# Kernel tuning notes

Measured on AMD Instinct MI355X. Metric: run time of the kernel, lower is better.

## Reference

```python
import jax, jax.numpy as jnp
import numpy as np

N = 16384        # num nodes
NE = 262144      # num edges (avg degree 16)
IN = 3           # input_dim
H = 128          # hidden_dim
ED = 2           # edge_dim (position differences, 2D coords)
L = 3            # num GNN layers
LAT = 64         # latent_dim
NR = 8192        # num reduced nodes (reduction_factor=0.5)
K = 3            # kNN for interpolation


def _ln(x, g, b, eps=1e-5):
    m = jnp.mean(x, axis=-1, keepdims=True)
    v = jnp.mean((x - m) ** 2, axis=-1, keepdims=True)
    return (x - m) / jnp.sqrt(v + eps) * g + b


def _mlp(x, w1, b1, w2, b2):
    return jax.nn.relu(x @ w1 + b1) @ w2 + b2


def setup_inputs() -> dict:
    key = jax.random.key(0)
    ks = jax.random.split(key, 32)
    def nrm(k, shape, s=0.05):
        return jax.random.normal(k, shape, dtype=jnp.float32) * s
    inp = {}
    inp["x"] = jax.random.normal(ks[0], (N, IN), dtype=jnp.float32)
    inp["node_positions"] = jax.random.uniform(ks[1], (N, 2), dtype=jnp.float32)
    inp["edge_index"] = jax.random.randint(ks[2], (2, NE), 0, N, dtype=jnp.int32)
    # mlp0 + lnm0
    inp["m0_w1"] = nrm(ks[3], (IN, H)); inp["m0_b1"] = jnp.zeros((H,), jnp.float32)
    inp["m0_w2"] = nrm(ks[4], (H, H)); inp["m0_b2"] = jnp.zeros((H,), jnp.float32)
    inp["ln0_g"] = jnp.ones((H,), jnp.float32); inp["ln0_b"] = jnp.zeros((H,), jnp.float32)
    # mlp1 + lnm1 (edge feature transform, edge_dim=2)
    inp["m1_w1"] = nrm(ks[5], (ED, H)); inp["m1_b1"] = jnp.zeros((H,), jnp.float32)
    inp["m1_w2"] = nrm(ks[6], (H, ED)); inp["m1_b2"] = jnp.zeros((ED,), jnp.float32)
    inp["ln1_g"] = jnp.ones((ED,), jnp.float32); inp["ln1_b"] = jnp.zeros((ED,), jnp.float32)
    # GNN layers (stacked over L)
    inp["g_msg_w1"] = nrm(ks[7], (L, 2 * H + ED, H)); inp["g_msg_b1"] = jnp.zeros((L, H), jnp.float32)
    inp["g_msg_w2"] = nrm(ks[8], (L, H, H)); inp["g_msg_b2"] = jnp.zeros((L, H), jnp.float32)
    inp["g_node_w1"] = nrm(ks[9], (L, 2 * H, H)); inp["g_node_b1"] = jnp.zeros((L, H), jnp.float32)
    inp["g_node_w2"] = nrm(ks[10], (L, H, H)); inp["g_node_b2"] = jnp.zeros((L, H), jnp.float32)
    inp["g_edge_w1"] = nrm(ks[11], (L, 2 * H + ED, H)); inp["g_edge_b1"] = jnp.zeros((L, H), jnp.float32)
    inp["g_edge_w2"] = nrm(ks[12], (L, H, ED)); inp["g_edge_b2"] = jnp.zeros((L, ED), jnp.float32)
    inp["g_lnn_g"] = jnp.ones((L, H), jnp.float32); inp["g_lnn_b"] = jnp.zeros((L, H), jnp.float32)
    inp["g_lne_g"] = jnp.ones((L, ED), jnp.float32); inp["g_lne_b"] = jnp.zeros((L, ED), jnp.float32)
    # mlp2 + lnm2
    inp["m2_w1"] = nrm(ks[13], (H, H)); inp["m2_b1"] = jnp.zeros((H,), jnp.float32)
    inp["m2_w2"] = nrm(ks[14], (H, H)); inp["m2_b2"] = jnp.zeros((H,), jnp.float32)
    inp["ln2_g"] = jnp.ones((H,), jnp.float32); inp["ln2_b"] = jnp.zeros((H,), jnp.float32)
    # output_proj
    inp["op_w1"] = nrm(ks[15], (H, H)); inp["op_b1"] = jnp.zeros((H,), jnp.float32)
    inp["op_w2"] = nrm(ks[16], (H, LAT)); inp["op_b2"] = jnp.zeros((LAT,), jnp.float32)
    return inp


def reference(x, edge_index, node_positions,
              m0_w1, m0_b1, m0_w2, m0_b2, ln0_g, ln0_b,
              m1_w1, m1_b1, m1_w2, m1_b2, ln1_g, ln1_b,
              g_msg_w1, g_msg_b1, g_msg_w2, g_msg_b2,
              g_node_w1, g_node_b1, g_node_w2, g_node_b2,
              g_edge_w1, g_edge_b1, g_edge_w2, g_edge_b2,
              g_lnn_g, g_lnn_b, g_lne_g, g_lne_b,
              m2_w1, m2_b1, m2_w2, m2_b2, ln2_g, ln2_b,
              op_w1, op_b1, op_w2, op_b2):
    row, col = edge_index[0], edge_index[1]
    # Stage 1: node encoder  U0 -> U1
    u = _ln(_mlp(x, m0_w1, m0_b1, m0_w2, m0_b2), ln0_g, ln0_b)
    # Stage 2: edge features from positions, E0 -> E1
    e = node_positions[col] - node_positions[row]          # [NE, 2]
    e = _ln(_mlp(e, m1_w1, m1_b1, m1_w2, m1_b2), ln1_g, ln1_b)
    # Stage 3: message-passing layers
    ones = jnp.ones((NE, 1), dtype=u.dtype)
    cnt = jnp.maximum(jax.ops.segment_sum(ones, col, num_segments=N), 1.0)
    for l in range(L):
        msg_in = jnp.concatenate([u[row], u[col], e], axis=-1)   # [NE, 2H+ED]
        m = _mlp(msg_in, g_msg_w1[l], g_msg_b1[l], g_msg_w2[l], g_msg_b2[l])
        agg = jax.ops.segment_sum(m, col, num_segments=N) / cnt  # mean aggregation
        u = _ln(u + _mlp(jnp.concatenate([u, agg], axis=-1),
                         g_node_w1[l], g_node_b1[l], g_node_w2[l], g_node_b2[l]),
                g_lnn_g[l], g_lnn_b[l])
        e = _ln(e + _mlp(jnp.concatenate([u[row], u[col], e], axis=-1),
                         g_edge_w1[l], g_edge_b1[l], g_edge_w2[l], g_edge_b2[l]),
                g_lne_g[l], g_lne_b[l])
    # Stage 4: U2 -> U3
    u3 = _ln(_mlp(u, m2_w1, m2_b1, m2_w2, m2_b2), ln2_g, ln2_b)
    # Stage 5: interpolate onto reduced coordinates (kNN inverse-distance weights)
    idx_r = jnp.floor(jnp.linspace(0.0, N - 1, NR)).astype(jnp.int32)
    x2 = node_positions[idx_r]                               # [NR, 2]
    d2 = (jnp.sum(x2 * x2, axis=1)[:, None]
          + jnp.sum(node_positions * node_positions, axis=1)[None, :]
          - 2.0 * x2 @ node_positions.T)                     # [NR, N]
    d2 = jnp.maximum(d2, 0.0)
    neg_d2, knn = jax.lax.top_k(-d2, K)                      # [NR, K]
    w = 1.0 / (jnp.sqrt(-neg_d2) + 1e-8)
    w = w / jnp.sum(w, axis=1, keepdims=True)
    z_feat = jnp.einsum('nk,nkh->nh', w, u3[knn])            # [NR, H]
    # Stage 6: global mean pool (no batch vector) + output projection
    z = jnp.mean(z_feat, axis=0, keepdims=True)              # [1, H]
    return _mlp(z, op_w1, op_b1, op_w2, op_b2)               # [1, LAT]
```

## Files before the change

kernel.cpp:

```cpp
#include <hip/hip_runtime.h>
#include <cfloat>

#define NN     16384
#define NEDGE  262144
#define HD     128
#define NLAYER 3
#define NRED   8192
#define LATD   64
#define GDIM   32

typedef __attribute__((ext_vector_type(8))) short short8;
typedef __attribute__((ext_vector_type(4))) float f32x4;

__device__ __forceinline__ unsigned short f2bf(float f) {
    union { float f; unsigned u; } v; v.f = f;
    unsigned u = v.u;
    unsigned r = u + 0x7fff + ((u >> 16) & 1);
    return (unsigned short)(r >> 16);
}
__device__ __forceinline__ void unp8(uint4 v, float* f) {
    unsigned w0=v.x, w1=v.y, w2=v.z, w3=v.w;
    f[0]=__uint_as_float(w0<<16); f[1]=__uint_as_float(w0&0xffff0000u);
    f[2]=__uint_as_float(w1<<16); f[3]=__uint_as_float(w1&0xffff0000u);
    f[4]=__uint_as_float(w2<<16); f[5]=__uint_as_float(w2&0xffff0000u);
// ... 113 lines not shown
        short8 a0 = *(const short8*)&HU.Hs[ 0 + lr][ks*32 + lq*8];
        short8 a1 = *(const short8*)&HU.Hs[16 + lr][ks*32 + lq*8];
        short8 a2 = *(const short8*)&HU.Hs[32 + lr][ks*32 + lq*8];
        short8 a3 = *(const short8*)&HU.Hs[48 + lr][ks*32 + lq*8];
        short8 b0 = *(const short8*)(W2p + (size_t)(((wave*2+0)*4 + ks)*64 + lane)*8);
        short8 b1v= *(const short8*)(W2p + (size_t)(((wave*2+1)*4 + ks)*64 + lane)*8);
        acc[0] = __builtin_amdgcn_mfma_f32_16x16x32_bf16(a0, b0, acc[0], 0,0,0);
        acc[1] = __builtin_amdgcn_mfma_f32_16x16x32_bf16(a0, b1v, acc[1], 0,0,0);
        acc[2] = __builtin_amdgcn_mfma_f32_16x16x32_bf16(a1, b0, acc[2], 0,0,0);
        acc[3] = __builtin_amdgcn_mfma_f32_16x16x32_bf16(a1, b1v, acc[3], 0,0,0);
        acc[4] = __builtin_amdgcn_mfma_f32_16x16x32_bf16(a2, b0, acc[4], 0,0,0);
        acc[5] = __builtin_amdgcn_mfma_f32_16x16x32_bf16(a2, b1v, acc[5], 0,0,0);
        acc[6] = __builtin_amdgcn_mfma_f32_16x16x32_bf16(a3, b0, acc[6], 0,0,0);
        acc[7] = __builtin_amdgcn_mfma_f32_16x16x32_bf16(a3, b1v, acc[7], 0,0,0);
    }
    #pragma unroll
    for (int b = 0; b < 2; ++b) {
        int n = (wave*2 + b)*16 + lr;
        float bb = B2[n];
        #pragma unroll
        for (int mt = 0; mt < 4; ++mt) {
            f32x4 v = acc[mt*2 + b];
            #pragma unroll
            for (int r = 0; r < 4; ++r) {
                int m = mt*16 + lq*4 + r;
                Rs[m][n] = v[r] + bb;
            }
        }
    }
    __syncthreads();
    {
        int m = tid >> 2, p = tid & 3;
        float s = 0.f;
        #pragma unroll 8
        for (int i = 0; i < 32; ++i) s += Rs[m][p*32 + i];
        red[m][p] = s;
    }
    __syncthreads();
    if (tid < 64) mstat[tid] = (red[tid][0]+red[tid][1]+red[tid][2]+red[tid][3]) * (1.f/HD);
    __syncthreads();
    {
        int m = tid >> 2, p = tid & 3;
        float mm = mstat[m];
        float s = 0.f;
        #pragma unroll 8
        for (int i = 0; i < 32; ++i) { float d = Rs[m][p*32 + i] - mm; s += d*d; }
        red[m][p] = s;
    }
    __syncthreads();
    if (tid < 64) sstat[tid] = sqrtf((red[tid][0]+red[tid][1]+red[tid][2]+red[tid][3]) * (1.f/HD) + 1e-5f);
    __syncthreads();
    for (int t = tid; t < 2048; t += 256) {
        int m = t >> 5, q = t & 31;
        int n = q*4;
        float mm = mstat[m], sd = sstat[m];
        float4 g4 = *(const float4*)(lg + n);
        float4 b4 = *(const float4*)(lb + n);
        float o0 = (Rs[m][n+0]-mm)/sd*g4.x + b4.x;
        float o1 = (Rs[m][n+1]-mm)/sd*g4.y + b4.y;
        float o2 = (Rs[m][n+2]-mm)/sd*g4.z + b4.z;
        float o3 = (Rs[m][n+3]-mm)/sd*g4.w + b4.w;
        float4 fo; fo.x=o0; fo.y=o1; fo.z=o2; fo.w=o3;
        *(float4*)(u + (size_t)(n0+m)*HD + n) = fo;
        uint2 pk; pk.x = f2bf(o0) | (f2bf(o1)<<16); pk.y = f2bf(o2) | (f2bf(o3)<<16);
        *(uint2*)(u16 + (size_t)(n0+m)*HD + n) = pk;
        int ksf = n >> 5, sub = (n >> 3) & 3;
        int slot = (ksf*4 + (m >> 4))*64 + ((m & 15) | (sub << 4));
        unsigned short* UF = (unsigned short*)HU.UF4;
        *(uint2*)&UF[slot*8 + (n & 7)] = pk;
    }
    __syncthreads();

    for (int g = 0; g < 2; ++g) {
        int ksOff = g*4;
        unsigned short* Out = g ? CM : RM;
        #pragma unroll
        for (int i = 0; i < 8; ++i) acc[i] = (f32x4){0.f,0.f,0.f,0.f};
        for (int ks = 0; ks < 4; ++ks) {
            short8 a0 = *(const short8*)&HU.UF4[(ks*4+0)*64 + lane];
            short8 a1 = *(const short8*)&HU.UF4[(ks*4+1)*64 + lane];
            short8 a2 = *(const short8*)&HU.UF4[(ks*4+2)*64 + lane];
            short8 a3 = *(const short8*)&HU.UF4[(ks*4+3)*64 + lane];
            short8 b0 = *(const short8*)(mW1p + (size_t)(((wave*2+0)*8 + ksOff + ks)*64 + lane)*8);
            short8 b1v= *(const short8*)(mW1p + (size_t)(((wave*2+1)*8 + ksOff + ks)*64 + lane)*8);
            acc[0] = __builtin_amdgcn_mfma_f32_16x16x32_bf16(a0, b0, acc[0], 0,0,0);
            acc[1] = __builtin_amdgcn_mfma_f32_16x16x32_bf16(a0, b1v, acc[1], 0,0,0);
            acc[2] = __builtin_amdgcn_mfma_f32_16x16x32_bf16(a1, b0, acc[2], 0,0,0);
            acc[3] = __builtin_amdgcn_mfma_f32_16x16x32_bf16(a1, b1v, acc[3], 0,0,0);
            acc[4] = __builtin_amdgcn_mfma_f32_16x16x32_bf16(a2, b0, acc[4], 0,0,0);
            acc[5] = __builtin_amdgcn_mfma_f32_16x16x32_bf16(a2, b1v, acc[5], 0,0,0);
            acc[6] = __builtin_amdgcn_mfma_f32_16x16x32_bf16(a3, b0, acc[6], 0,0,0);
            acc[7] = __builtin_amdgcn_mfma_f32_16x16x32_bf16(a3, b1v, acc[7], 0,0,0);
        }
        #pragma unroll
        for (int b = 0; b < 2; ++b) {
            int n = (wave*2 + b)*16 + lr;
            float bb = g ? mB1[n] : 0.f;
            #pragma unroll
            for (int mt = 0; mt < 4; ++mt) {
                f32x4 v = acc[mt*2 + b];
                #pragma unroll
                for (int r = 0; r < 4; ++r) {
                    int rowp = n0 + mt*16 + lq*4 + r;
                    unsigned hv = f2bf(v[r] + bb);
                    unsigned ph = (unsigned)__shfl_xor((int)hv, 1, 64);
                    if (!(lr & 1))
                        *(unsigned*)&Out[(size_t)rowp*HD + n] = hv | (ph << 16);
                }
            }
        }
    }
}

__global__ __launch_bounds__(256) void k_edge_enc(
    const float* __restrict__ pos, const int* __restrict__ row, const int* __restrict__ col,
    const float* __restrict__ w1, const float* __restrict__ b1,
    const float* __restrict__ w2, const float* __restrict__ b2,
    const float* __restrict__ lg, const float* __restrict__ lb,
    float* __restrict__ ef)
{
    int e = blockIdx.x*256 + threadIdx.x;
    if (e >= NEDGE) return;
    int r = row[e], c = col[e];
    float e0 = pos[c*2]   - pos[r*2];
    float e1 = pos[c*2+1] - pos[r*2+1];
    float o0 = b2[0], o1 = b2[1];
    for (int j = 0; j < HD; ++j) {
        float h = fmaxf(e0*w1[j] + e1*w1[HD+j] + b1[j], 0.f);
        o0 += h*w2[j*2];
        o1 += h*w2[j*2+1];
    }
    float m  = 0.5f*(o0 + o1);
    float d0 = o0 - m, d1 = o1 - m;
    float v  = 0.5f*(d0*d0 + d1*d1);
    float sd = sqrtf(v + 1e-5f);
    ef[e*2]   = d0/sd*lg[0] + lb[0];
    ef[e*2+1] = d1/sd*lg[1] + lb[1];
}

__global__ void k_count2(const int* __restrict__ col, const float* __restrict__ pos,
                         int* __restrict__ cnt, int* __restrict__ gcnt)
{
    int e = blockIdx.x*256 + threadIdx.x;
    if (e < NEDGE) atomicAdd(&cnt[col[e]], 1);
    if (e < NN) {
        int cx = min(max((int)(pos[e*2]  *(float)GDIM), 0), GDIM-1);
        int cy = min(max((int)(pos[e*2+1]*(float)GDIM), 0), GDIM-1);
        atomicAdd(&gcnt[cy*GDIM + cx], 1);
    }
}

__global__ __launch_bounds__(256) void k_scan2(
    const int* __restrict__ cnt, int* __restrict__ head,
    const int* __restrict__ gcnt, int* __restrict__ gstart, int* __restrict__ ghead,
    float* __restrict__ zsum)
{
    __shared__ int ls[257];
    int tid = threadIdx.x;
    if (blockIdx.x == 0) {
        int base = tid * (NN/256);
        int s = 0;
        for (int i = 0; i < NN/256; ++i) s += cnt[base + i];
        ls[tid+1] = s;
        if (tid == 0) ls[0] = 0;
        __syncthreads();
        if (tid == 0) for (int i = 1; i <= 256; ++i) ls[i] += ls[i-1];
        __syncthreads();
        int run = ls[tid];
        for (int i = 0; i < NN/256; ++i) {
            head[base + i] = run;
            run += cnt[base + i];
        }
    } else {
        if (tid < HD) zsum[tid] = 0.f;
        int base = tid * 4;
        int s = 0;
        for (int i = 0; i < 4; ++i) s += gcnt[base + i];
        ls[tid+1] = s;
        if (tid == 0) ls[0] = 0;
        __syncthreads();
        if (tid == 0) for (int i = 1; i <= 256; ++i) ls[i] += ls[i-1];
        __syncthreads();
        int run = ls[tid];
        for (int i = 0; i < 4; ++i) {
            gstart[base+i] = run; ghead[base+i] = run;
            run += gcnt[base+i];
        }
        if (tid == 255) gstart[GDIM*GDIM] = run;
    }
}

__global__ __launch_bounds__(256) void k_scatter2(
    const int* __restrict__ col, const float* __restrict__ pos,
    int* __restrict__ head, int* __restrict__ perm,
    int* __restrict__ ghead, float2* __restrict__ psort, int* __restrict__ pidx)
{
    int e = blockIdx.x*256 + threadIdx.x;
    if (e < NEDGE) {
        int p = atomicAdd(&head[col[e]], 1);
        perm[p] = e;
    }
    if (e < NN) {
        float px = pos[e*2], py = pos[e*2+1];
        int cx = min(max((int)(px*(float)GDIM), 0), GDIM-1);
        int cy = min(max((int)(py*(float)GDIM), 0), GDIM-1);
        int p = atomicAdd(&ghead[cy*GDIM + cx], 1);
        float2 pp; pp.x = px; pp.y = py;
        psort[p] = pp;
        pidx[p] = e;
    }
}

__global__ __launch_bounds__(256) void k_knnsel(
    const float* __restrict__ pos, const int* __restrict__ gstart,
    const float2* __restrict__ psort, const int* __restrict__ pidx,
    int* __restrict__ knnidx, float* __restrict__ knnw)
{
    int r = blockIdx.x*256 + threadIdx.x;
    int ni = (int)(2.0*r + (double)r/8191.0);
    float qx = pos[ni*2], qy = pos[ni*2+1];
    float s2 = qx*qx + qy*qy;
    int cx = min(max((int)(qx*(float)GDIM), 0), GDIM-1);
    int cy = min(max((int)(qy*(float)GDIM), 0), GDIM-1);
    const float h = 1.f/(float)GDIM;
    unsigned long long k0 = ~0ull, k1 = ~0ull, k2 = ~0ull;
    for (int rr = 0; rr < GDIM; ++rr) {
        if (rr > 0 && k2 != ~0ull) {
            float bound = rr*h;
            float d3 = __uint_as_float((unsigned)(k2 >> 32));
            if (d3 < bound*bound*0.9999f) break;
        }
        int ylo = max(cy-rr, 0), yhi = min(cy+rr, GDIM-1);
        int xlo = max(cx-rr, 0), xhi = min(cx+rr, GDIM-1);
        for (int gy = ylo; gy <= yhi; ++gy) {
            bool yedge = (gy == cy-rr) || (gy == cy+rr);
            for (int gx = xlo; gx <= xhi; ++gx) {
                if (!yedge && gx != cx-rr && gx != cx+rr) continue;
                int cell = gy*GDIM + gx;
                int s = gstart[cell], e = gstart[cell+1];
                for (; s < e; ++s) {
                    float2 p = psort[s];
                    float sc = p.x*p.x + p.y*p.y;
                    float dt = qx*p.x + qy*p.y;
                    float d2 = fmaxf(s2 + sc - 2.f*dt, 0.f);
                    unsigned long long key =
                        ((unsigned long long)__float_as_uint(d2) << 32) | (unsigned)pidx[s];
                    unsigned long long a0 = umin64(k0, key);
                    unsigned long long a1 = umin64(k1, umax64(k0, key));
                    unsigned long long a2 = umin64(k2, umax64(k1, key));
                    k0 = a0; k1 = a1; k2 = a2;
                }
            }
        }
    }
    float d0 = __uint_as_float((unsigned)(k0 >> 32));
    float d1 = __uint_as_float((unsigned)(k1 >> 32));
    float d2 = __uint_as_float((unsigned)(k2 >> 32));
    float w0 = 1.f/(sqrtf(d0) + 1e-8f);
    float w1 = 1.f/(sqrtf(d1) + 1e-8f);
    float w2 = 1.f/(sqrtf(d2) + 1e-8f);
    float ws = w0 + w1 + w2;
    knnidx[r*3+0] = (int)(unsigned)(k0 & 0xffffffffu);
    knnidx[r*3+1] = (int)(unsigned)(k1 & 0xffffffffu);
    knnidx[r*3+2] = (int)(unsigned)(k2 & 0xffffffffu);
    knnw[r*3+0] = w0/ws;
    knnw[r*3+1] = w1/ws;
    knnw[r*3+2] = w2/ws;
}

__global__ __launch_bounds__(256) void k_gather(
    const float* __restrict__ u3, const int* __restrict__ knnidx,
    const float* __restrict__ knnw, float* __restrict__ zsum)
{
    __shared__ float zp[HD];
    int tid = threadIdx.x;
    if (tid < HD) zp[tid] = 0.f;
    __syncthreads();
    int lane = tid & 63, w = tid >> 6;
    int q = blockIdx.x*4 + w;
    int i0 = knnidx[q*3], i1 = knnidx[q*3+1], i2 = knnidx[q*3+2];
    float w0 = knnw[q*3], w1 = knnw[q*3+1], w2 = knnw[q*3+2];
    const float* r0 = u3 + (size_t)i0*HD;
    const float* r1 = u3 + (size_t)i1*HD;
    const float* r2 = u3 + (size_t)i2*HD;
    for (int c = lane; c < HD; c += 64) {
        float v = w0*r0[c] + w1*r1[c] + w2*r2[c];
        atomicAdd(&zp[c], v);
    }
    __syncthreads();
    if (tid < HD) atomicAdd(&zsum[tid], zp[tid]);
}

__global__ __launch_bounds__(256) void k_hagg0(
    const unsigned short* __restrict__ RM, const unsigned short* __restrict__ CM,
    const float* __restrict__ ef,
    const int* __restrict__ row, const int* __restrict__ col,
    const int* __restrict__ perm,
    const float* __restrict__ mW1e,
    float* __restrict__ agg)
{
    __shared__ float Ms[64][132];
    __shared__ float Pw[256];
    __shared__ float Es[64][2];
    __shared__ int colS[64], rowS[64], eS[64];
    int tid = threadIdx.x;
    int e0  = blockIdx.x * 64;
    if (tid < 64) {
        int e = perm[e0 + tid];
        eS[tid] = e; colS[tid] = col[e]; rowS[tid] = row[e];
    }
    for (int t = tid; t < 256; t += 256) Pw[t] = mW1e[t];
    __syncthreads();
    if (tid < 128) { Es[tid>>1][tid&1] = ef[(size_t)eS[tid>>1]*2 + (tid&1)]; }
    __syncthreads();

    int mP = (tid >> 6)*16 + (tid & 15);
    int ccB = ((tid & 63) >> 4)*8;
    float e0v = Es[mP][0], e1v = Es[mP][1];
    #pragma unroll
    for (int s4 = 0; s4 < 4; ++s4) {
        int cc = s4*32 + ccB;
        uint4 ra = *(const uint4*)(RM + (size_t)rowS[mP]*HD + cc);
        uint4 cb = *(const uint4*)(CM + (size_t)colS[mP]*HD + cc);
        float rf[8], cf[8];
        unp8(ra, rf); unp8(cb, cf);
        float4 o0, o1;
        o0.x = fmaxf(rf[0]+cf[0]+e0v*Pw[cc+0]+e1v*Pw[128+cc+0], 0.f);
        o0.y = fmaxf(rf[1]+cf[1]+e0v*Pw[cc+1]+e1v*Pw[128+cc+1], 0.f);
        o0.z = fmaxf(rf[2]+cf[2]+e0v*Pw[cc+2]+e1v*Pw[128+cc+2], 0.f);
        o0.w = fmaxf(rf[3]+cf[3]+e0v*Pw[cc+3]+e1v*Pw[128+cc+3], 0.f);
        o1.x = fmaxf(rf[4]+cf[4]+e0v*Pw[cc+4]+e1v*Pw[128+cc+4], 0.f);
        o1.y = fmaxf(rf[5]+cf[5]+e0v*Pw[cc+5]+e1v*Pw[128+cc+5], 0.f);
        o1.z = fmaxf(rf[6]+cf[6]+e0v*Pw[cc+6]+e1v*Pw[128+cc+6], 0.f);
        o1.w = fmaxf(rf[7]+cf[7]+e0v*Pw[cc+7]+e1v*Pw[128+cc+7], 0.f);
        *(float4*)&Ms[mP][cc]   = o0;
        *(float4*)&Ms[mP][cc+4] = o1;
    }
    __syncthreads();

    {
        int n = tid & 127, hh = tid >> 7;
        int m0 = hh*32;
        float accv = 0.f;
        int cur = colS[m0];
        for (int m = m0; m < m0 + 32; ++m) {
            int cm = colS[m];
            if (cm != cur) {
                atomicAdd(&agg[(size_t)cur*HD + n], accv);
                accv = 0.f; cur = cm;
            }
            accv += Ms[m][n];
        }
        atomicAdd(&agg[(size_t)cur*HD + n], accv);
    }
}

union MsHFu { uint4 HF4[1024]; float Ms[64][132]; };

__global__ __launch_bounds__(256) void k_edgemsg2(
    const unsigned short* __restrict__ RE, const unsigned short* __restrict__ CE,
    const unsigned short* __restrict__ RM, const unsigned short* __restrict__ CM,
    float* __restrict__ ef,
    const int* __restrict__ row, const int* __restrict__ col,
    const int* __restrict__ perm,
    const float* __restrict__ eW1e,
    const unsigned short* __restrict__ eW2p, const float* __restrict__ eB2,
    const float* __restrict__ elg, const float* __restrict__ elb,
    const float* __restrict__ mW1e,
    float* __restrict__ agg, int writeEf)
{
    __shared__ MsHFu MU;
    __shared__ float Pew[256], Pmw[256];
    __shared__ float Es[64][2];
    __shared__ int colS[64], rowS[64], eS[64];
    int tid = threadIdx.x;
    int e0  = blockIdx.x * 64;
    if (tid < 64) {
        int e = perm[e0 + tid];
        eS[tid] = e; colS[tid] = col[e]; rowS[tid] = row[e];
    }
    for (int t = tid; t < 256; t += 256) { Pew[t] = eW1e[t]; Pmw[t] = mW1e[t]; }
    __syncthreads();

    int mP = (tid >> 6)*16 + (tid & 15);
    int ccB = ((tid & 63) >> 4)*8;
    uint4 regR[4], regC[4];
    #pragma unroll
    for (int s4 = 0; s4 < 4; ++s4) {
        int cc = s4*32 + ccB;
        regR[s4] = *(const uint4*)(RM + (size_t)rowS[mP]*HD + cc);
        regC[s4] = *(const uint4*)(CM + (size_t)colS[mP]*HD + cc);
    }
    if (tid < 128) { Es[tid>>1][tid&1] = ef[(size_t)eS[tid>>1]*2 + (tid&1)]; }
    __syncthreads();

    int lane = tid & 63, wave = tid >> 6;
    int lr = lane & 15, lq = lane >> 4;

    {
        float e0v = Es[mP][0], e1v = Es[mP][1];
        #pragma unroll
        for (int s4 = 0; s4 < 4; ++s4) {
            int s = tid + s4*256;
            int cc = s4*32 + ccB;
            uint4 ra = *(const uint4*)(RE + (size_t)rowS[mP]*HD + cc);
            uint4 cb = *(const uint4*)(CE + (size_t)colS[mP]*HD + cc);
            float rf[8], cf[8];
            unp8(ra, rf); unp8(cb, cf);
            unsigned short hb[8];
            #pragma unroll
            for (int j = 0; j < 8; ++j) {
                int n = cc + j;
                float o = rf[j] + cf[j] + e0v*Pew[n] + e1v*Pew[128+n];
                hb[j] = f2bf(fmaxf(o, 0.f));
            }
            uint4 pk;
            pk.x = hb[0] | ((unsigned)hb[1]<<16); pk.y = hb[2] | ((unsigned)hb[3]<<16);
            pk.z = hb[4] | ((unsigned)hb[5]<<16); pk.w = hb[6] | ((unsigned)hb[7]<<16);
            MU.HF4[s] = pk;
        }
    }
    __syncthreads();

    f32x4 a2 = (f32x4){0.f,0.f,0.f,0.f};
    for (int ks = 0; ks < 4; ++ks) {
        short8 a = *(const short8*)&MU.HF4[(ks*4 + wave)*64 + lane];
        short8 b = *(const short8*)(eW2p + (size_t)(ks*64 + lane)*8);
        a2 = __builtin_amdgcn_mfma_f32_16x16x32_bf16(a, b, a2, 0,0,0);
    }
    if (lr < 2) {
        int d = lr;
        float bb = eB2[d];
        float gg = elg[d], bl = elb[d];
        #pragma unroll
        for (int r = 0; r < 4; ++r) {
            int m = wave*16 + lq*4 + r;
            float rv = Es[m][d] + a2[r] + bb;
            float other = __shfl_xor(rv, 1, 64);
            float mm = 0.5f*(rv + other);
            float dr = rv - mm, dro = other - mm;
            float vv = 0.5f*(dr*dr + dro*dro);
            float outv = dr / sqrtf(vv + 1e-5f) * gg + bl;
            Es[m][d] = outv;
// ... 147 lines not shown
        acc[3] = __builtin_amdgcn_mfma_f32_16x16x32_bf16(a1, b1, acc[3], 0,0,0);
        acc[4] = __builtin_amdgcn_mfma_f32_16x16x32_bf16(a2, b0, acc[4], 0,0,0);
        acc[5] = __builtin_amdgcn_mfma_f32_16x16x32_bf16(a2, b1, acc[5], 0,0,0);
        acc[6] = __builtin_amdgcn_mfma_f32_16x16x32_bf16(a3, b0, acc[6], 0,0,0);
        acc[7] = __builtin_amdgcn_mfma_f32_16x16x32_bf16(a3, b1, acc[7], 0,0,0);
    }
    #pragma unroll
    for (int b = 0; b < 2; ++b) {
        int n = (wave*2 + b)*16 + lr;
        float bb = B1[n];
        #pragma unroll
        for (int mt = 0; mt < 4; ++mt) {
            f32x4 v = acc[mt*2 + b];
            #pragma unroll
            for (int r = 0; r < 4; ++r) {
                int m = mt*16 + lq*4 + r;
                HU.Hs[m][n] = f2bf(fmaxf(v[r] + bb, 0.f));
            }
        }
    }
    __syncthreads();

    #pragma unroll
    for (int i = 0; i < 8; ++i) acc[i] = (f32x4){0.f,0.f,0.f,0.f};
    for (int ks = 0; ks < 4; ++ks) {
        short8 a0 = *(const short8*)&HU.Hs[ 0 + lr][ks*32 + lq*8];
        short8 a1 = *(const short8*)&HU.Hs[16 + lr][ks*32 + lq*8];
        short8 a2 = *(const short8*)&HU.Hs[32 + lr][ks*32 + lq*8];
        short8 a3 = *(const short8*)&HU.Hs[48 + lr][ks*32 + lq*8];
        short8 b0 = *(const short8*)(W2p + (size_t)(((wave*2+0)*4 + ks)*64 + lane)*8);
        short8 b1 = *(const short8*)(W2p + (size_t)(((wave*2+1)*4 + ks)*64 + lane)*8);
        acc[0] = __builtin_amdgcn_mfma_f32_16x16x32_bf16(a0, b0, acc[0], 0,0,0);
        acc[1] = __builtin_amdgcn_mfma_f32_16x16x32_bf16(a0, b1, acc[1], 0,0,0);
        acc[2] = __builtin_amdgcn_mfma_f32_16x16x32_bf16(a1, b0, acc[2], 0,0,0);
        acc[3] = __builtin_amdgcn_mfma_f32_16x16x32_bf16(a1, b1, acc[3], 0,0,0);
        acc[4] = __builtin_amdgcn_mfma_f32_16x16x32_bf16(a2, b0, acc[4], 0,0,0);
        acc[5] = __builtin_amdgcn_mfma_f32_16x16x32_bf16(a2, b1, acc[5], 0,0,0);
        acc[6] = __builtin_amdgcn_mfma_f32_16x16x32_bf16(a3, b0, acc[6], 0,0,0);
        acc[7] = __builtin_amdgcn_mfma_f32_16x16x32_bf16(a3, b1, acc[7], 0,0,0);
    }
    #pragma unroll
    for (int b = 0; b < 2; ++b) {
        int n = (wave*2 + b)*16 + lr;
        float bb = B2[n];
        #pragma unroll
        for (int mt = 0; mt < 4; ++mt) {
            f32x4 v = acc[mt*2 + b];
            #pragma unroll
            for (int r = 0; r < 4; ++r) {
                int m = mt*16 + lq*4 + r;
                XR.Rs[m][n] = u[(size_t)(n0+m)*HD + n] + v[r] + bb;
            }
        }
    }
    __syncthreads();
    {
        int m = tid >> 2, p = tid & 3;
        float s = 0.f;
        #pragma unroll 8
        for (int i = 0; i < 32; ++i) s += XR.Rs[m][p*32 + i];
        red[m][p] = s;
    }
    __syncthreads();
    if (tid < 64) mstat[tid] = (red[tid][0]+red[tid][1]+red[tid][2]+red[tid][3]) * (1.f/HD);
    __syncthreads();
    {
        int m = tid >> 2, p = tid & 3;
        float mm = mstat[m];
        float s = 0.f;
        #pragma unroll 8
        for (int i = 0; i < 32; ++i) { float d = XR.Rs[m][p*32 + i] - mm; s += d*d; }
        red[m][p] = s;
    }
    __syncthreads();
    if (tid < 64) sstat[tid] = sqrtf((red[tid][0]+red[tid][1]+red[tid][2]+red[tid][3]) * (1.f/HD) + 1e-5f);
    __syncthreads();
    for (int t = tid; t < 2048; t += 256) {
        int m = t >> 5, q = t & 31;
        int n = q*4;
        float mm = mstat[m], sd = sstat[m];
        float4 g4 = *(const float4*)(lg + n);
        float4 b4 = *(const float4*)(lb + n);
        float o0 = (XR.Rs[m][n+0]-mm)/sd*g4.x + b4.x;
        float o1 = (XR.Rs[m][n+1]-mm)/sd*g4.y + b4.y;
        float o2 = (XR.Rs[m][n+2]-mm)/sd*g4.z + b4.z;
        float o3 = (XR.Rs[m][n+3]-mm)/sd*g4.w + b4.w;
        float4 fo; fo.x=o0; fo.y=o1; fo.z=o2; fo.w=o3;
        *(float4*)(u + (size_t)(n0+m)*HD + n) = fo;
        uint2 pk; pk.x = f2bf(o0) | (f2bf(o1)<<16); pk.y = f2bf(o2) | (f2bf(o3)<<16);
        *(uint2*)(u16 + (size_t)(n0+m)*HD + n) = pk;
        if (doExtra) {
            int ksf = n >> 5, sub = (n >> 3) & 3;
            int slot = (ksf*4 + (m >> 4))*64 + ((m & 15) | (sub << 4));
            unsigned short* UF = (unsigned short*)HU.UF4;
            *(uint2*)&UF[slot*8 + (n & 7)] = pk;
        }
    }
    {
        float4 z; z.x=0.f; z.y=0.f; z.z=0.f; z.w=0.f;
        for (int t = tid; t < 2048; t += 256)
            *(float4*)(agg + (size_t)(n0 + (t>>5))*HD + (t&31)*4) = z;
    }
    if (!doExtra) return;
    __syncthreads();

    for (int g = 0; g < 4; ++g) {
        const unsigned short* Bp = (g < 2) ? eW1p : mW1pN;
        int ksOff = (g & 1) * 4;
        unsigned short* Out = (g == 0) ? RE : (g == 1) ? CE : (g == 2) ? RM : CM;
        const float* bias = (g == 1) ? eB1c : (g == 3) ? mB1N : (const float*)nullptr;
        #pragma unroll
        for (int i = 0; i < 8; ++i) acc[i] = (f32x4){0.f,0.f,0.f,0.f};
        for (int ks = 0; ks < 4; ++ks) {
            short8 a0 = *(const short8*)&HU.UF4[(ks*4+0)*64 + lane];
            short8 a1 = *(const short8*)&HU.UF4[(ks*4+1)*64 + lane];
            short8 a2 = *(const short8*)&HU.UF4[(ks*4+2)*64 + lane];
            short8 a3 = *(const short8*)&HU.UF4[(ks*4+3)*64 + lane];
            short8 b0 = *(const short8*)(Bp + (size_t)(((wave*2+0)*8 + ksOff + ks)*64 + lane)*8);
            short8 b1 = *(const short8*)(Bp + (size_t)(((wave*2+1)*8 + ksOff + ks)*64 + lane)*8);
            acc[0] = __builtin_amdgcn_mfma_f32_16x16x32_bf16(a0, b0, acc[0], 0,0,0);
            acc[1] = __builtin_amdgcn_mfma_f32_16x16x32_bf16(a0, b1, acc[1], 0,0,0);
            acc[2] = __builtin_amdgcn_mfma_f32_16x16x32_bf16(a1, b0, acc[2], 0,0,0);
            acc[3] = __builtin_amdgcn_mfma_f32_16x16x32_bf16(a1, b1, acc[3], 0,0,0);
            acc[4] = __builtin_amdgcn_mfma_f32_16x16x32_bf16(a2, b0, acc[4], 0,0,0);
            acc[5] = __builtin_amdgcn_mfma_f32_16x16x32_bf16(a2, b1, acc[5], 0,0,0);
            acc[6] = __builtin_amdgcn_mfma_f32_16x16x32_bf16(a3, b0, acc[6], 0,0,0);
            acc[7] = __builtin_amdgcn_mfma_f32_16x16x32_bf16(a3, b1, acc[7], 0,0,0);
        }
        #pragma unroll
        for (int b = 0; b < 2; ++b) {
            int n = (wave*2 + b)*16 + lr;
            float bb = bias ? bias[n] : 0.f;
            #pragma unroll
            for (int mt = 0; mt < 4; ++mt) {
                f32x4 v = acc[mt*2 + b];
                #pragma unroll
                for (int r = 0; r < 4; ++r) {
                    int rowp = n0 + mt*16 + lq*4 + r;
                    unsigned hv = f2bf(v[r] + bb);
                    unsigned ph = (unsigned)__shfl_xor((int)hv, 1, 64);
                    if (!(lr & 1))
                        *(unsigned*)&Out[(size_t)rowp*HD + n] = hv | (ph << 16);
                }
            }
        }
    }
}

__global__ __launch_bounds__(256) void k_m2_mfma(
    const unsigned short* __restrict__ u16,
    const unsigned short* __restrict__ W1p, const float* __restrict__ B1,
    const unsigned short* __restrict__ W2p, const float* __restrict__ B2,
    const float* __restrict__ lg, const float* __restrict__ lb,
    float* __restrict__ u3)
{
    __shared__ unsigned short Xs[64][136];
    __shared__ unsigned short Hs[64][136];
    __shared__ float Rs[64][132];
    __shared__ float red[64][4];
    __shared__ float mstat[64], sstat[64];
    int tid = threadIdx.x;
    int n0  = blockIdx.x * 64;
    for (int t = tid; t < 1024; t += 256) {
        int el = t >> 4, kc = t & 15;
        uint4 v = *(const uint4*)(u16 + (size_t)(n0+el)*HD + kc*8);
        *(uint4*)&Xs[el][kc*8] = v;
    }
    __syncthreads();

    int lane = tid & 63, wave = tid >> 6;
    int lr = lane & 15, lq = lane >> 4;
    f32x4 acc[8];
    #pragma unroll
    for (int i = 0; i < 8; ++i) acc[i] = (f32x4){0.f,0.f,0.f,0.f};
    for (int ks = 0; ks < 4; ++ks) {
        short8 a0 = *(const short8*)&Xs[ 0 + lr][ks*32 + lq*8];
        short8 a1 = *(const short8*)&Xs[16 + lr][ks*32 + lq*8];
        short8 a2 = *(const short8*)&Xs[32 + lr][ks*32 + lq*8];
        short8 a3 = *(const short8*)&Xs[48 + lr][ks*32 + lq*8];
        short8 b0 = *(const short8*)(W1p + (size_t)(((wave*2+0)*4 + ks)*64 + lane)*8);
        short8 b1 = *(const short8*)(W1p + (size_t)(((wave*2+1)*4 + ks)*64 + lane)*8);
        acc[0] = __builtin_amdgcn_mfma_f32_16x16x32_bf16(a0, b0, acc[0], 0,0,0);
        acc[1] = __builtin_amdgcn_mfma_f32_16x16x32_bf16(a0, b1, acc[1], 0,0,0);
        acc[2] = __builtin_amdgcn_mfma_f32_16x16x32_bf16(a1, b0, acc[2], 0,0,0);
        acc[3] = __builtin_amdgcn_mfma_f32_16x16x32_bf16(a1, b1, acc[3], 0,0,0);
        acc[4] = __builtin_amdgcn_mfma_f32_16x16x32_bf16(a2, b0, acc[4], 0,0,0);
        acc[5] = __builtin_amdgcn_mfma_f32_16x16x32_bf16(a2, b1, acc[5], 0,0,0);
        acc[6] = __builtin_amdgcn_mfma_f32_16x16x32_bf16(a3, b0, acc[6], 0,0,0);
        acc[7] = __builtin_amdgcn_mfma_f32_16x16x32_bf16(a3, b1, acc[7], 0,0,0);
    }
    #pragma unroll
    for (int b = 0; b < 2; ++b) {
        int n = (wave*2 + b)*16 + lr;
        float bb = B1[n];
        #pragma unroll
        for (int mt = 0; mt < 4; ++mt) {
            f32x4 v = acc[mt*2 + b];
            #pragma unroll
            for (int r = 0; r < 4; ++r) {
                int m = mt*16 + lq*4 + r;
                Hs[m][n] = f2bf(fmaxf(v[r] + bb, 0.f));
            }
        }
    }
    __syncthreads();

    #pragma unroll
    for (int i = 0; i < 8; ++i) acc[i] = (f32x4){0.f,0.f,0.f,0.f};
    for (int ks = 0; ks < 4; ++ks) {
        short8 a0 = *(const short8*)&Hs[ 0 + lr][ks*32 + lq*8];
        short8 a1 = *(const short8*)&Hs[16 + lr][ks*32 + lq*8];
        short8 a2 = *(const short8*)&Hs[32 + lr][ks*32 + lq*8];
        short8 a3 = *(const short8*)&Hs[48 + lr][ks*32 + lq*8];
        short8 b0 = *(const short8*)(W2p + (size_t)(((wave*2+0)*4 + ks)*64 + lane)*8);
        short8 b1 = *(const short8*)(W2p + (size_t)(((wave*2+1)*4 + ks)*64 + lane)*8);
        acc[0] = __builtin_amdgcn_mfma_f32_16x16x32_bf16(a0, b0, acc[0], 0,0,0);
        acc[1] = __builtin_amdgcn_mfma_f32_16x16x32_bf16(a0, b1, acc[1], 0,0,0);
        acc[2] = __builtin_amdgcn_mfma_f32_16x16x32_bf16(a1, b0, acc[2], 0,0,0);
        acc[3] = __builtin_amdgcn_mfma_f32_16x16x32_bf16(a1, b1, acc[3], 0,0,0);
        acc[4] = __builtin_amdgcn_mfma_f32_16x16x32_bf16(a2, b0, acc[4], 0,0,0);
        acc[5] = __builtin_amdgcn_mfma_f32_16x16x32_bf16(a2, b1, acc[5], 0,0,0);
        acc[6] = __builtin_amdgcn_mfma_f32_16x16x32_bf16(a3, b0, acc[6], 0,0,0);
        acc[7] = __builtin_amdgcn_mfma_f32_16x16x32_bf16(a3, b1, acc[7], 0,0,0);
    }
    #pragma unroll
    for (int b = 0; b < 2; ++b) {
        int n = (wave*2 + b)*16 + lr;
        float bb = B2[n];
        #pragma unroll
        for (int mt = 0; mt < 4; ++mt) {
            f32x4 v = acc[mt*2 + b];
            #pragma unroll
            for (int r = 0; r < 4; ++r) {
                int m = mt*16 + lq*4 + r;
                Rs[m][n] = v[r] + bb;
            }
        }
    }
    __syncthreads();
    {
        int m = tid >> 2, p = tid & 3;
        float s = 0.f;
        #pragma unroll 8
        for (int i = 0; i < 32; ++i) s += Rs[m][p*32 + i];
        red[m][p] = s;
    }
    __syncthreads();
    if (tid < 64) mstat[tid] = (red[tid][0]+red[tid][1]+red[tid][2]+red[tid][3]) * (1.f/HD);
    __syncthreads();
    {
        int m = tid >> 2, p = tid & 3;
        float mm = mstat[m];
        float s = 0.f;
        #pragma unroll 8
        for (int i = 0; i < 32; ++i) { float d = Rs[m][p*32 + i] - mm; s += d*d; }
        red[m][p] = s;
    }
    __syncthreads();
    if (tid < 64) sstat[tid] = sqrtf((red[tid][0]+red[tid][1]+red[tid][2]+red[tid][3]) * (1.f/HD) + 1e-5f);
    __syncthreads();
    for (int t = tid; t < 2048; t += 256) {
        int m = t >> 5, q = t & 31;
        int n = q*4;
        float mm = mstat[m], sd = sstat[m];
        float4 g4 = *(const float4*)(lg + n);
        float4 b4 = *(const float4*)(lb + n);
        float4 fo;
        fo.x = (Rs[m][n+0]-mm)/sd*g4.x + b4.x;
        fo.y = (Rs[m][n+1]-mm)/sd*g4.y + b4.y;
        fo.z = (Rs[m][n+2]-mm)/sd*g4.z + b4.z;
        fo.w = (Rs[m][n+3]-mm)/sd*g4.w + b4.w;
        *(float4*)(u3 + (size_t)(n0+m)*HD + n) = fo;
    }
}

__global__ __launch_bounds__(128) void k_out(
    const float* __restrict__ zsum,
    const float* __restrict__ w1, const float* __restrict__ b1,
    const float* __restrict__ w2, const float* __restrict__ b2,
    float* __restrict__ out)
{
    __shared__ float zs[HD];
    __shared__ float hs[HD];
    int j = threadIdx.x;
    zs[j] = zsum[j] * (1.f/NRED);
    __syncthreads();
    float o = b1[j];
    #pragma unroll 8
    for (int k = 0; k < HD; ++k) o += zs[k]*w1[k*HD + j];
    hs[j] = fmaxf(o, 0.f);
    __syncthreads();
    if (j < LATD) {
        float o2 = b2[j];
        #pragma unroll 8
        for (int k = 0; k < HD; ++k) o2 += hs[k]*w2[k*LATD + j];
        out[j] = o2;
    }
}

extern "C" void kernel_launch(void* const* d_in, const int* in_sizes, int n_in,
                              void* d_out, int out_size, void* d_ws, size_t ws_size,
                              hipStream_t stream)
{
    const float* x    = (const float*)d_in[0];
    const float* pos  = (const float*)d_in[1];
    const int*   eidx = (const int*)d_in[2];
    const int* row = eidx;
    const int* col = eidx + NEDGE;
    const float* m0_w1 = (const float*)d_in[3];
    const float* m0_b1 = (const float*)d_in[4];
    const float* m0_w2 = (const float*)d_in[5];
    const float* m0_b2 = (const float*)d_in[6];
    const float* ln0_g = (const float*)d_in[7];
    const float* ln0_b = (const float*)d_in[8];
    const float* m1_w1 = (const float*)d_in[9];
    const float* m1_b1 = (const float*)d_in[10];
    const float* m1_w2 = (const float*)d_in[11];
    const float* m1_b2 = (const float*)d_in[12];
    const float* ln1_g = (const float*)d_in[13];
    const float* ln1_b = (const float*)d_in[14];
    const float* g_msg_w1  = (const float*)d_in[15];
    const float* g_msg_b1  = (const float*)d_in[16];
    const float* g_msg_w2  = (const float*)d_in[17];
    const float* g_msg_b2  = (const float*)d_in[18];
    const float* g_node_w1 = (const float*)d_in[19];
    const float* g_node_b1 = (const float*)d_in[20];
    const float* g_node_w2 = (const float*)d_in[21];
    const float* g_node_b2 = (const float*)d_in[22];
    const float* g_edge_w1 = (const float*)d_in[23];
    const float* g_edge_b1 = (const float*)d_in[24];
    const float* g_edge_w2 = (const float*)d_in[25];
    const float* g_edge_b2 = (const float*)d_in[26];
    const float* g_lnn_g   = (const float*)d_in[27];
    const float* g_lnn_b   = (const float*)d_in[28];
    const float* g_lne_g   = (const float*)d_in[29];
    const float* g_lne_b   = (const float*)d_in[30];
    const float* m2_w1 = (const float*)d_in[31];
    const float* m2_b1 = (const float*)d_in[32];
    const float* m2_w2 = (const float*)d_in[33];
    const float* m2_b2 = (const float*)d_in[34];
    const float* ln2_g = (const float*)d_in[35];
    const float* ln2_b = (const float*)d_in[36];
    const float* op_w1 = (const float*)d_in[37];
    const float* op_b1 = (const float*)d_in[38];
    const float* op_w2 = (const float*)d_in[39];
    const float* op_b2 = (const float*)d_in[40];

    float* u    = (float*)d_ws;
    float* ef   = u + (size_t)NN*HD;
    float* agg  = ef + (size_t)NEDGE*2;
    int*   cnt  = (int*)(agg + (size_t)NN*HD);
    int*   gcnt = cnt + NN;
    int*   head = gcnt + 1024;
    int*   perm = head + NN;
    float* zsum = (float*)(perm + NEDGE);
    int*   gstart = (int*)(zsum + HD);
    int*   ghead  = gstart + 1026;
    int*   pidx   = ghead + 1024;
    int*   knnidx = pidx + NN;
    float2* psort = (float2*)(knnidx + NRED*3 + 2);
    float* knnw   = (float*)(psort + NN);
    unsigned short* u16 = (unsigned short*)(knnw + NRED*3 + 1);
    unsigned short* packs = u16 + (size_t)NN*HD;
    unsigned short* msgW1p  = packs;
    unsigned short* msgW2p  = packs + 98304;
    unsigned short* edgeW1p = packs + 147456;
    unsigned short* nodeW1p = packs + 245760;
    unsigned short* nodeW2p = packs + 344064;
    unsigned short* edgeW2p = packs + 393216;
    unsigned short* m0w2p   = packs + 399360;
    unsigned short* m2w1p   = packs + 415744;
    unsigned short* m2w2p   = packs + 432128;
    unsigned short* RE = packs + PK_TOTAL;
    unsigned short* CE = RE + (size_t)NN*HD;
    unsigned short* RM = CE + (size_t)NN*HD;
    unsigned short* CM = RM + (size_t)NN*HD;
    float* u3 = agg;

    k_pack_all<<<(PK_TOTAL + 255)/256, 256, 0, stream>>>(
        g_msg_w1, g_msg_w2, g_edge_w1, g_node_w1, g_node_w2, g_edge_w2,
        m0_w2, m2_w1, m2_w2, packs);

    hipMemsetAsync(cnt, 0, (NN + 1024)*sizeof(int), stream);

    k_nenc_mfma<<<NN/64, 256, 0, stream>>>(x, m0_w1, m0_b1, m0w2p, m0_b2, ln0_g, ln0_b,
                                           msgW1p, g_msg_b1, u, u16, RM, CM, agg);
    k_edge_enc<<<NEDGE/256, 256, 0, stream>>>(pos, row, col, m1_w1, m1_b1, m1_w2, m1_b2,
                                              ln1_g, ln1_b, ef);

    k_count2<<<NEDGE/256, 256, 0, stream>>>(col, pos, cnt, gcnt);
    k_scan2<<<2, 256, 0, stream>>>(cnt, head, gcnt, gstart, ghead, zsum);
    k_scatter2<<<NEDGE/256, 256, 0, stream>>>(col, pos, head, perm, ghead, psort, pidx);
    k_knnsel<<<NRED/256, 256, 0, stream>>>(pos, gstart, psort, pidx, knnidx, knnw);

    k_hagg0<<<NEDGE/64, 256, 0, stream>>>(RM, CM, ef, row, col, perm,
        g_msg_w1 + 256*HD, agg);
    k_node_mfma<<<NN/64, 256, 0, stream>>>(u, u16, agg, cnt,
        nodeW1p, g_node_b1, nodeW2p, g_node_b2, g_lnn_g, g_lnn_b,
        msgW2p, g_msg_b2,
        1, edgeW1p + 0*32768, g_edge_b1 + 0*HD, msgW1p + 1*32768, g_msg_b1 + 1*HD,
        RE, CE, RM, CM);

    for (int l = 0; l < NLAYER-1; ++l) {
        k_edgemsg2<<<NEDGE/64, 256, 0, stream>>>(RE, CE, RM, CM, ef, row, col, perm,
            g_edge_w1 + (size_t)l*258*HD + 256*HD,
            edgeW2p + l*2048, g_edge_b2 + l*2, g_lne_g + l*2, g_lne_b + l*2,
            g_msg_w1 + (size_t)(l+1)*258*HD + 256*HD,
            agg, (l == 0) ? 1 : 0);
        int doExtra = (l == 0) ? 1 : 0;
        k_node_mfma<<<NN/64, 256, 0, stream>>>(u, u16, agg, cnt,
            nodeW1p + (l+1)*32768, g_node_b1 + (l+1)*HD,
            nodeW2p + (l+1)*16384, g_node_b2 + (l+1)*HD,
            g_lnn_g + (l+1)*HD, g_lnn_b + (l+1)*HD,
            msgW2p + (l+1)*16384, g_msg_b2 + (l+1)*HD,
            doExtra, edgeW1p + 1*32768, g_edge_b1 + 1*HD, msgW1p + 2*32768, g_msg_b1 + 2*HD,
            RE, CE, RM, CM);
    }

    k_m2_mfma<<<NN/64, 256, 0, stream>>>(u16, m2w1p, m2_b1, m2w2p, m2_b2, ln2_g, ln2_b, u3);
    k_gather<<<NRED/4, 256, 0, stream>>>(u3, knnidx, knnw, zsum);
    k_out<<<1, 128, 0, stream>>>(zsum, op_w1, op_b1, op_w2, op_b2, (float*)d_out);
}
```

Before: 494.4 us.

## Fold kNN interpolation and mean pool into per-node coefficients fused with m2

Because the final output only needs the mean of the interpolated features, the kNN step now scatters each normalized weight into a per-node coefficient array. The m2 kernel multiplies each LayerNorm output row by its coefficient and reduces per block into partial sums, which k_out adds up. This removes the u3 write, the separate gather kernel and the global float atomics on zsum. The cost is float atomics on coef, a 256-way serial sum in the single-block output kernel, and a different summation order.

```diff
diff --git a/kernel.cpp b/kernel.cpp
--- a/kernel.cpp
+++ b/kernel.cpp
@@ -289,8 +289,7 @@
 
 __global__ __launch_bounds__(256) void k_scan2(
     const int* __restrict__ cnt, int* __restrict__ head,
-    const int* __restrict__ gcnt, int* __restrict__ gstart, int* __restrict__ ghead,
-    float* __restrict__ zsum)
+    const int* __restrict__ gcnt, int* __restrict__ gstart, int* __restrict__ ghead)
 {
     __shared__ int ls[257];
     int tid = threadIdx.x;
@@ -309,7 +308,6 @@
             run += cnt[base + i];
         }
     } else {
-        if (tid < HD) zsum[tid] = 0.f;
         int base = tid * 4;
         int s = 0;
         for (int i = 0; i < 4; ++i) s += gcnt[base + i];
@@ -351,7 +349,7 @@
 __global__ __launch_bounds__(256) void k_knnsel(
     const float* __restrict__ pos, const int* __restrict__ gstart,
     const float2* __restrict__ psort, const int* __restrict__ pidx,
-    int* __restrict__ knnidx, float* __restrict__ knnw)
+    float* __restrict__ coef)
 {
     int r = blockIdx.x*256 + threadIdx.x;
     int ni = (int)(2.0*r + (double)r/8191.0);
@@ -397,35 +395,9 @@
     float w1 = 1.f/(sqrtf(d1) + 1e-8f);
     float w2 = 1.f/(sqrtf(d2) + 1e-8f);
     float ws = w0 + w1 + w2;
-    knnidx[r*3+0] = (int)(unsigned)(k0 & 0xffffffffu);
-    knnidx[r*3+1] = (int)(unsigned)(k1 & 0xffffffffu);
-    knnidx[r*3+2] = (int)(unsigned)(k2 & 0xffffffffu);
-    knnw[r*3+0] = w0/ws;
-    knnw[r*3+1] = w1/ws;
-    knnw[r*3+2] = w2/ws;
-}
-
-__global__ __launch_bounds__(256) void k_gather(
-    const float* __restrict__ u3, const int* __restrict__ knnidx,
-    const float* __restrict__ knnw, float* __restrict__ zsum)
-{
-    __shared__ float zp[HD];
-    int tid = threadIdx.x;
-    if (tid < HD) zp[tid] = 0.f;
-    __syncthreads();
-    int lane = tid & 63, w = tid >> 6;
-    int q = blockIdx.x*4 + w;
-    int i0 = knnidx[q*3], i1 = knnidx[q*3+1], i2 = knnidx[q*3+2];
-    float w0 = knnw[q*3], w1 = knnw[q*3+1], w2 = knnw[q*3+2];
-    const float* r0 = u3 + (size_t)i0*HD;
-    const float* r1 = u3 + (size_t)i1*HD;
-    const float* r2 = u3 + (size_t)i2*HD;
-    for (int c = lane; c < HD; c += 64) {
-        float v = w0*r0[c] + w1*r1[c] + w2*r2[c];
-        atomicAdd(&zp[c], v);
-    }
-    __syncthreads();
-    if (tid < HD) atomicAdd(&zsum[tid], zp[tid]);
+    atomicAdd(&coef[(int)(unsigned)(k0 & 0xffffffffu)], w0/ws);
+    atomicAdd(&coef[(int)(unsigned)(k1 & 0xffffffffu)], w1/ws);
+    atomicAdd(&coef[(int)(unsigned)(k2 & 0xffffffffu)], w2/ws);
 }
 
 __global__ __launch_bounds__(256) void k_hagg0(
@@ -879,15 +851,17 @@
     const unsigned short* __restrict__ W1p, const float* __restrict__ B1,
     const unsigned short* __restrict__ W2p, const float* __restrict__ B2,
     const float* __restrict__ lg, const float* __restrict__ lb,
-    float* __restrict__ u3)
+    const float* __restrict__ coef, float* __restrict__ partial)
 {
     __shared__ unsigned short Xs[64][136];
     __shared__ unsigned short Hs[64][136];
     __shared__ float Rs[64][132];
     __shared__ float red[64][4];
     __shared__ float mstat[64], sstat[64];
+    __shared__ float zp[HD];
     int tid = threadIdx.x;
     int n0  = blockIdx.x * 64;
+    if (tid < HD) zp[tid] = 0.f;
     for (int t = tid; t < 1024; t += 256) {
         int el = t >> 4, kc = t & 15;
         uint4 v = *(const uint4*)(u16 + (size_t)(n0+el)*HD + kc*8);
@@ -986,23 +960,33 @@
     __syncthreads();
     if (tid < 64) sstat[tid] = sqrtf((red[tid][0]+red[tid][1]+red[tid][2]+red[tid][3]) * (1.f/HD) + 1e-5f);
     __syncthreads();
-    for (int t = tid; t < 2048; t += 256) {
-        int m = t >> 5, q = t & 31;
+    {
+        float4 a4; a4.x=0.f; a4.y=0.f; a4.z=0.f; a4.w=0.f;
+        int q = tid & 31;
         int n = q*4;
-        float mm = mstat[m], sd = sstat[m];
         float4 g4 = *(const float4*)(lg + n);
         float4 b4 = *(const float4*)(lb + n);
-        float4 fo;
-        fo.x = (Rs[m][n+0]-mm)/sd*g4.x + b4.x;
-        fo.y = (Rs[m][n+1]-mm)/sd*g4.y + b4.y;
-        fo.z = (Rs[m][n+2]-mm)/sd*g4.z + b4.z;
-        fo.w = (Rs[m][n+3]-mm)/sd*g4.w + b4.w;
-        *(float4*)(u3 + (size_t)(n0+m)*HD + n) = fo;
-    }
+        for (int t = tid; t < 2048; t += 256) {
+            int m = t >> 5;
+            float mm = mstat[m], sd = sstat[m];
+            float cw = coef[n0 + m];
+            float o0 = (Rs[m][n+0]-mm)/sd*g4.x + b4.x;
+            float o1 = (Rs[m][n+1]-mm)/sd*g4.y + b4.y;
+            float o2 = (Rs[m][n+2]-mm)/sd*g4.z + b4.z;
+            float o3 = (Rs[m][n+3]-mm)/sd*g4.w + b4.w;
+            a4.x += cw*o0; a4.y += cw*o1; a4.z += cw*o2; a4.w += cw*o3;
+        }
+        atomicAdd(&zp[n+0], a4.x);
+        atomicAdd(&zp[n+1], a4.y);
+        atomicAdd(&zp[n+2], a4.z);
+        atomicAdd(&zp[n+3], a4.w);
+    }
+    __syncthreads();
+    if (tid < HD) partial[(size_t)blockIdx.x*HD + tid] = zp[tid];
 }
 
 __global__ __launch_bounds__(128) void k_out(
-    const float* __restrict__ zsum,
+    const float* __restrict__ partial,
     const float* __restrict__ w1, const float* __restrict__ b1,
     const float* __restrict__ w2, const float* __restrict__ b2,
     float* __restrict__ out)
@@ -1010,7 +994,9 @@
     __shared__ float zs[HD];
     __shared__ float hs[HD];
     int j = threadIdx.x;
-    zs[j] = zsum[j] * (1.f/NRED);
+    float s = 0.f;
+    for (int p = 0; p < NN/64; ++p) s += partial[(size_t)p*HD + j];
+    zs[j] = s * (1.f/NRED);
     __syncthreads();
     float o = b1[j];
     #pragma unroll 8
@@ -1078,16 +1064,15 @@
     float* agg  = ef + (size_t)NEDGE*2;
     int*   cnt  = (int*)(agg + (size_t)NN*HD);
     int*   gcnt = cnt + NN;
-    int*   head = gcnt + 1024;
+    float* coef = (float*)(gcnt + 1024);
+    int*   head = (int*)(coef + NN);
     int*   perm = head + NN;
-    float* zsum = (float*)(perm + NEDGE);
-    int*   gstart = (int*)(zsum + HD);
+    float* partial = (float*)(perm + NEDGE);
+    int*   gstart = (int*)(partial + (NN/64)*HD);
     int*   ghead  = gstart + 1026;
     int*   pidx   = ghead + 1024;
-    int*   knnidx = pidx + NN;
-    float2* psort = (float2*)(knnidx + NRED*3 + 2);
-    float* knnw   = (float*)(psort + NN);
-    unsigned short* u16 = (unsigned short*)(knnw + NRED*3 + 1);
+    float2* psort = (float2*)(pidx + NN);
+    unsigned short* u16 = (unsigned short*)(psort + NN);
     unsigned short* packs = u16 + (size_t)NN*HD;
     unsigned short* msgW1p  = packs;
     unsigned short* msgW2p  = packs + 98304;
@@ -1102,13 +1087,12 @@
     unsigned short* CE = RE + (size_t)NN*HD;
     unsigned short* RM = CE + (size_t)NN*HD;
     unsigned short* CM = RM + (size_t)NN*HD;
-    float* u3 = agg;
 
     k_pack_all<<<(PK_TOTAL + 255)/256, 256, 0, stream>>>(
         g_msg_w1, g_msg_w2, g_edge_w1, g_node_w1, g_node_w2, g_edge_w2,
         m0_w2, m2_w1, m2_w2, packs);
 
-    hipMemsetAsync(cnt, 0, (NN + 1024)*sizeof(int), stream);
+    hipMemsetAsync(cnt, 0, (NN + 1024 + NN)*sizeof(int), stream);
 
     k_nenc_mfma<<<NN/64, 256, 0, stream>>>(x, m0_w1, m0_b1, m0w2p, m0_b2, ln0_g, ln0_b,
                                            msgW1p, g_msg_b1, u, u16, RM, CM, agg);
@@ -1116,9 +1100,9 @@
                                               ln1_g, ln1_b, ef);
 
     k_count2<<<NEDGE/256, 256, 0, stream>>>(col, pos, cnt, gcnt);
-    k_scan2<<<2, 256, 0, stream>>>(cnt, head, gcnt, gstart, ghead, zsum);
+    k_scan2<<<2, 256, 0, stream>>>(cnt, head, gcnt, gstart, ghead);
     k_scatter2<<<NEDGE/256, 256, 0, stream>>>(col, pos, head, perm, ghead, psort, pidx);
-    k_knnsel<<<NRED/256, 256, 0, stream>>>(pos, gstart, psort, pidx, knnidx, knnw);
+    k_knnsel<<<NRED/256, 256, 0, stream>>>(pos, gstart, psort, pidx, coef);
 
     k_hagg0<<<NEDGE/64, 256, 0, stream>>>(RM, CM, ef, row, col, perm,
         g_msg_w1 + 256*HD, agg);
@@ -1144,7 +1128,7 @@
             RE, CE, RM, CM);
     }
 
-    k_m2_mfma<<<NN/64, 256, 0, stream>>>(u16, m2w1p, m2_b1, m2w2p, m2_b2, ln2_g, ln2_b, u3);
-    k_gather<<<NRED/4, 256, 0, stream>>>(u3, knnidx, knnw, zsum);
-    k_out<<<1, 128, 0, stream>>>(zsum, op_w1, op_b1, op_w2, op_b2, (float*)d_out);
-}
+    k_m2_mfma<<<NN/64, 256, 0, stream>>>(u16, m2w1p, m2_b1, m2w2p, m2_b2, ln2_g, ln2_b,
+                                         coef, partial);
+    k_out<<<1, 128, 0, stream>>>(partial, op_w1, op_b1, op_w2, op_b2, (float*)d_out);
+}
```

After: 450.0 us (median of 2 runs). 1.1x faster.
